# Performance work log

Measured on AMD Instinct MI355X. Metric: run time of the kernel, lower is better.

The kernel has to match this reference:

```python
import jax, jax.numpy as jnp
import numpy as np

N = 131072          # num MCMC chains (num_samples)
N_STEPS = 60        # sample_mcmc default n_steps
EPS_INIT = 10.0     # sample_mcmc default eps_init
H = 128             # hidden width of the energy MLP


def setup_inputs() -> dict:
    key = jax.random.key(0)
    ks = jax.random.split(key, 8)
    d = {}
    # init points uniform in [-1, 1] (mimics the fresh-sample branch / buffer contents)
    d["x0"] = jax.random.uniform(ks[0], (N, 2), jnp.float32, minval=-1.0, maxval=1.0)
    # MLP 2 -> 128 -> 128 -> 128 -> 128 -> 1 (Kaiming-ish scale)
    def init_w(k, shape):
        fan_in = shape[0]
        return jax.random.normal(k, shape, jnp.float32) / jnp.sqrt(jnp.float32(fan_in))
    d["w1"] = init_w(ks[1], (2, H));  d["b1"] = jnp.zeros((H,), jnp.float32)
    d["w2"] = init_w(ks[2], (H, H));  d["b2"] = jnp.zeros((H,), jnp.float32)
    d["w3"] = init_w(ks[3], (H, H));  d["b3"] = jnp.zeros((H,), jnp.float32)
    d["w4"] = init_w(ks[4], (H, H));  d["b4"] = jnp.zeros((H,), jnp.float32)
    d["w5"] = init_w(ks[5], (H, 1));  d["b5"] = jnp.zeros((1,), jnp.float32)
    # pre-drawn Langevin noise for each of the 60 steps (torch.randn_like per step)
    d["noise"] = jax.random.normal(ks[6], (N_STEPS, N, 2), jnp.float32)
    return d


def _energy(x, params):
    # nn.Sequential(Linear, SiLU, Linear, SiLU, Linear, SiLU, Linear, SiLU, Linear)
    w1, b1, w2, b2, w3, b3, w4, b4, w5, b5 = params
    h = jax.nn.silu(x @ w1 + b1)
    h = jax.nn.silu(h @ w2 + b2)
    h = jax.nn.silu(h @ w3 + b3)
    h = jax.nn.silu(h @ w4 + b4)
    return h @ w5 + b5  # [N, 1]


def reference(x0, w1, b1, w2, b2, w3, b3, w4, b4, w5, b5, noise):
    params = (w1, b1, w2, b2, w3, b3, w4, b4, w5, b5)
    # grad of sum of energies wrt x == per-sample dE/dx
    grad_fn = jax.grad(lambda x: _energy(x, params).sum())

    def step(x, inp):
        i, nz = inp
        eps = EPS_INIT * (1.0 - i / N_STEPS)  # eps_init - eps_init*step/n_steps
        # torch.autograd.grad (create_graph=False) -> detached grad
        g = jnp.clip(jax.lax.stop_gradient(grad_fn(x)), -0.03, 0.03)
        x = jnp.clip(x + jnp.sqrt(2.0 * eps) * nz * 0.005 + eps * g, -2.43, 3.05)
        return x, None

    steps = jnp.arange(N_STEPS, dtype=jnp.float32)
    x, _ = jax.lax.scan(step, x0, (steps, noise))
    return x
```

## Files before the change

### kernel.cpp

```cpp
#include <hip/hip_runtime.h>
#include <stdint.h>

#define NTOT    131072
#define NSTEP   60
#define SBLK    32
#define NBLK    (NTOT / SBLK)
#define PLANE_H 16384
#define IMG_H   32768
#define BPLANE_H 4096
#define ACT_H   8192

#define OFF_ACT0 0
#define OFF_ACT1 16384
#define OFF_GP   32768
#define OFF_W1C  33792
#define OFF_B2   35840
#define OFF_B3   36352
#define OFF_B4   36864
#define OFF_W5   37376
#define OFF_XB   37888
#define LDS_TOTAL 38144

typedef float  f32x4  __attribute__((ext_vector_type(4)));
typedef float  f32x16 __attribute__((ext_vector_type(16)));
typedef short  bf16x8 __attribute__((ext_vector_type(8)));
union FragU { bf16x8 v; uint32_t u[4]; uint16_t h[8]; };

static __device__ __forceinline__ uint32_t rne_bits(float f) {
  uint32_t u = __float_as_uint(f);
  return u + 0x7fffu + ((u >> 16) & 1u);
}
static __device__ __forceinline__ float fsigm(float z) {
  return __builtin_amdgcn_rcpf(1.0f + __builtin_amdgcn_exp2f(z * -1.44269504089f));
}
static __device__ __forceinline__ uint32_t cvt_pk_bf16(float a, float b) {
  uint32_t r;
  asm("v_cvt_pk_bf16_f32 %0, %1, %2" : "=v"(r) : "v"(a), "v"(b));
  return r;
}

extern "C" __global__ void ebm_prep_kernel(const float* __restrict__ w2,
                                           const float* __restrict__ w3,
                                           const float* __restrict__ w4,
                                           uint16_t* __restrict__ ws) {
  int img = blockIdx.x;
  bool bwd = img >= 3;
  int li = bwd ? 5 - img : img;
  const float* w = (li == 0) ? w2 : (li == 1) ? w3 : w4;
  uint16_t* hiP = ws + (size_t)img * IMG_H;
  uint16_t* loP = hiP + PLANE_H;
  for (int e = threadIdx.x; e < 16384; e += blockDim.x) {
    int i = e >> 7, o = e & 127;
    int m = bwd ? i : o;
    int k = bwd ? o : i;
    int slot = ((m >> 5) * 8 + (k >> 4)) * 64 + (m & 31) + 32 * ((k >> 3) & 1);
    int off = slot * 8 + (k & 7);
    float v = w[e];
    uint32_t tb = rne_bits(v);
    float lo = v - __uint_as_float(tb & 0xffff0000u);
    hiP[off] = (uint16_t)(tb >> 16);
    loP[off] = (uint16_t)(rne_bits(lo) >> 16);
  }
}

extern "C" __global__ void __launch_bounds__(256, 2)
ebm_mcmc_kernel(const float* __restrict__ x0, const float* __restrict__ w1,
                const float* __restrict__ b1, const float* __restrict__ b2,
                const float* __restrict__ b3, const float* __restrict__ b4,
                const float* __restrict__ w5, const float* __restrict__ noise,
                const uint16_t* __restrict__ wsW, float* __restrict__ out)
{
  extern __shared__ char smem[];
  uint16_t* ACT0  = (uint16_t*)(smem + OFF_ACT0);
  uint16_t* ACT1  = (uint16_t*)(smem + OFF_ACT1);
  float*    GPf   = (float*)(smem + OFF_GP);
  f32x4*    W1C   = (f32x4*)(smem + OFF_W1C);
  float*    B2s   = (float*)(smem + OFF_B2);
  float*    B3s   = (float*)(smem + OFF_B3);
  float*    B4s   = (float*)(smem + OFF_B4);
  float*    W5s   = (float*)(smem + OFF_W5);
  float*    XB    = (float*)(smem + OFF_XB);

  const int t   = threadIdx.x;
  const int blk = blockIdx.x;

  if (t < 128) {
    f32x4 v; v.x = w1[t]; v.y = w1[128 + t]; v.z = b1[t]; v.w = 0.0f;
    W1C[t] = v;
    B2s[t] = b2[t]; B3s[t] = b3[t]; B4s[t] = b4[t]; W5s[t] = w5[t];
  }
  if (t < 64) XB[t] = x0[(size_t)blk * 64 + t];

  const int lane = t & 63;
  const int wave = t >> 6;
  const int c32 = lane & 31;
  const int h   = lane >> 5;
  const int wr  = wave;

  size_t nbase = (size_t)blk * 64 + (t & 63);
  float nz = (t < 64) ? noise[nbase] : 0.0f;

  __syncthreads();

  f32x16 acc;
  float D1[16], D2[16], D3[16];

  auto gemm = [&](int img, const uint16_t* AB) {
    const uint16_t* ab = wsW + (size_t)img * IMG_H + (size_t)(wr * 4096 + lane * 8);
    acc = (f32x16)0.0f;
#pragma unroll
    for (int ks = 0; ks < 8; ++ks) {
      FragU Ah, Al;
      Ah.v = *(const bf16x8*)(ab + ks * 512);
      Al.v = *(const bf16x8*)(ab + ks * 512 + PLANE_H);
      const uint16_t* bp = AB + (ks * 64 + lane) * 8;
      FragU Bh, Bl;
      Bh.v = *(const bf16x8*)bp;
      Bl.v = *(const bf16x8*)(bp + BPLANE_H);
      acc = __builtin_amdgcn_mfma_f32_32x32x16_bf16(Ah.v, Bh.v, acc, 0, 0, 0);
      acc = __builtin_amdgcn_mfma_f32_32x32x16_bf16(Ah.v, Bl.v, acc, 0, 0, 0);
      acc = __builtin_amdgcn_mfma_f32_32x32x16_bf16(Al.v, Bh.v, acc, 0, 0, 0);
    }
  };

  auto storeAct = [&](uint16_t* AB, int tt, f32x4 v) {
    uint32_t h01 = cvt_pk_bf16(v[0], v[1]);
    uint32_t h23 = cvt_pk_bf16(v[2], v[3]);
    float r0 = v[0] - __uint_as_float(h01 << 16);
    float r1 = v[1] - __uint_as_float(h01 & 0xffff0000u);
    float r2 = v[2] - __uint_as_float(h23 << 16);
    float r3 = v[3] - __uint_as_float(h23 & 0xffff0000u);
    int slot = (2 * wr + (tt >> 1)) * 64 + c32 + 32 * (tt & 1);
    uint16_t* p = AB + slot * 8 + 4 * h;
    *(uint2*)p = make_uint2(h01, h23);
    *(uint2*)(p + BPLANE_H) = make_uint2(cvt_pk_bf16(r0, r1), cvt_pk_bf16(r2, r3));
  };

  auto ep_fwd = [&](const float* Bs, float* D, uint16_t* AB) {
#pragma unroll
    for (int tt = 0; tt < 4; ++tt) {
      f32x4 bv = *(const f32x4*)(Bs + 32 * wr + 8 * tt + 4 * h);
      f32x4 hv;
#pragma unroll
      for (int rr = 0; rr < 4; ++rr) {
        float z = acc[4 * tt + rr] + bv[rr];
        float s = fsigm(z);
        float hh = z * s;
        D[4 * tt + rr] = s * (1.0f + z - hh);
        hv[rr] = hh;
      }
      storeAct(AB, tt, hv);
    }
  };

  auto ep_v4 = [&](uint16_t* AB) {
#pragma unroll
    for (int tt = 0; tt < 4; ++tt) {
      f32x4 bv = *(const f32x4*)(B4s + 32 * wr + 8 * tt + 4 * h);
      f32x4 wv = *(const f32x4*)(W5s + 32 * wr + 8 * tt + 4 * h);
      f32x4 vv;
#pragma unroll
      for (int rr = 0; rr < 4; ++rr) {
        float z = acc[4 * tt + rr] + bv[rr];
        float s = fsigm(z);
        vv[rr] = wv[rr] * (s * (1.0f + z - z * s));
      }
      storeAct(AB, tt, vv);
    }
  };

  auto ep_bwd = [&](float* D, uint16_t* AB) {
#pragma unroll
    for (int tt = 0; tt < 4; ++tt) {
      f32x4 vv;
#pragma unroll
      for (int rr = 0; rr < 4; ++rr)
        vv[rr] = acc[4 * tt + rr] * D[4 * tt + rr];
      storeAct(AB, tt, vv);
    }
  };

  auto ep_bwd1 = [&]() {
    float gx = 0.f, gy = 0.f;
#pragma unroll
    for (int tt = 0; tt < 4; ++tt) {
      const f32x4* wp = W1C + 32 * wr + 8 * tt + 4 * h;
#pragma unroll
      for (int rr = 0; rr < 4; ++rr) {
        f32x4 w = wp[rr];
        float v = acc[4 * tt + rr] * D1[4 * tt + rr];
        gx = fmaf(v, w.x, gx);
        gy = fmaf(v, w.y, gy);
      }
    }
    gx += __shfl_xor(gx, 32);
    gy += __shfl_xor(gy, 32);
    if (h == 0) {
      *(float2*)(GPf + (wr * 32 + c32) * 2) = make_float2(gx, gy);
    }
  };

  auto l1_phase = [&](uint16_t* AB) {
    float2 xv = *(const float2*)(XB + 2 * c32);
#pragma unroll
    for (int tt = 0; tt < 4; ++tt) {
      const f32x4* wp = W1C + 32 * wr + 8 * tt + 4 * h;
      f32x4 hv;
#pragma unroll
      for (int rr = 0; rr < 4; ++rr) {
        f32x4 w = wp[rr];
        float z = fmaf(xv.x, w.x, fmaf(xv.y, w.y, w.z));
        float s = fsigm(z);
        float hh = z * s;
        D1[4 * tt + rr] = s * (1.0f + z - hh);
        hv[rr] = hh;
      }
      storeAct(AB, tt, hv);
    }
  };

  auto g_finish = [&](int step) {
    if (t < 64) {
      float g = GPf[t] + GPf[64 + t] + GPf[128 + t] + GPf[192 + t];
      g = fminf(fmaxf(g, -0.03f), 0.03f);
      float epsv = 10.0f * (1.0f - (float)step / 60.0f);
      float xn = XB[t] + sqrtf(2.0f * epsv) * nz * 0.005f + epsv * g;
      xn = fminf(fmaxf(xn, -2.43f), 3.05f);
      XB[t] = xn;
      if (step == NSTEP - 1) {
        out[(size_t)blk * 64 + t] = xn;
      } else {
        nz = noise[(size_t)(step + 1) * NTOT * 2 + nbase];
      }
    }
  };

#pragma unroll 1
  for (int step = 0; step < NSTEP; ++step) {
    l1_phase(ACT0);                 __syncthreads();
    gemm(0, ACT0); ep_fwd(B2s, D2, ACT1); __syncthreads();
    gemm(1, ACT1); ep_fwd(B3s, D3, ACT0); __syncthreads();
    gemm(2, ACT0); ep_v4(ACT1);           __syncthreads();
    gemm(3, ACT1); ep_bwd(D3, ACT0);      __syncthreads();
    gemm(4, ACT0); ep_bwd(D2, ACT1);      __syncthreads();
    gemm(5, ACT1); ep_bwd1();             __syncthreads();
    g_finish(step);                 __syncthreads();
  }
}

extern "C" void kernel_launch(void* const* d_in, const int* in_sizes, int n_in,
                              void* d_out, int out_size, void* d_ws, size_t ws_size,
                              hipStream_t stream) {
  (void)in_sizes; (void)n_in; (void)out_size; (void)ws_size;
  hipFuncSetAttribute((const void*)ebm_mcmc_kernel,
                      hipFuncAttributeMaxDynamicSharedMemorySize, LDS_TOTAL);
  ebm_prep_kernel<<<6, 256, 0, stream>>>(
      (const float*)d_in[3], (const float*)d_in[5], (const float*)d_in[7],
      (uint16_t*)d_ws);
  ebm_mcmc_kernel<<<NBLK, 256, LDS_TOTAL, stream>>>(
      (const float*)d_in[0], (const float*)d_in[1], (const float*)d_in[2],
      (const float*)d_in[4], (const float*)d_in[6], (const float*)d_in[8],
      (const float*)d_in[9], (const float*)d_in[11], (const uint16_t*)d_ws,
      (float*)d_out);
}
```

Before: 5.862 ms.

## Process 64 chains per block so each weight fragment feeds two MFMA tiles

Doubles the samples per block from 32 to 64. Each wave now keeps two accumulator tiles, so every A-fragment (weight) loaded from global memory is reused across two B tiles, which halves weight traffic per sample and the number of blocks. It also recomputes the layer-1 SiLU derivative in the last backward epilogue instead of keeping D1 in registers. In exchange it doubles LDS use and accumulator registers, which may lower occupancy.

Result: slower. 6.268 ms (+6.9%).

```diff
diff --git a/kernel.cpp b/kernel.cpp
--- a/kernel.cpp
+++ b/kernel.cpp
@@ -3,23 +3,22 @@
 
 #define NTOT    131072
 #define NSTEP   60
-#define SBLK    32
+#define SBLK    64
 #define NBLK    (NTOT / SBLK)
 #define PLANE_H 16384
 #define IMG_H   32768
-#define BPLANE_H 4096
-#define ACT_H   8192
+#define BPLANE_H 8192
 
 #define OFF_ACT0 0
-#define OFF_ACT1 16384
-#define OFF_GP   32768
-#define OFF_W1C  33792
-#define OFF_B2   35840
-#define OFF_B3   36352
-#define OFF_B4   36864
-#define OFF_W5   37376
-#define OFF_XB   37888
-#define LDS_TOTAL 38144
+#define OFF_ACT1 32768
+#define OFF_GP   65536
+#define OFF_W1C  67584
+#define OFF_B2   69632
+#define OFF_B3   70144
+#define OFF_B4   70656
+#define OFF_W5   71168
+#define OFF_XB   71680
+#define LDS_TOTAL 72192
 
 typedef float  f32x4  __attribute__((ext_vector_type(4)));
 typedef float  f32x16 __attribute__((ext_vector_type(16)));
@@ -88,8 +87,8 @@
     f32x4 v; v.x = w1[t]; v.y = w1[128 + t]; v.z = b1[t]; v.w = 0.0f;
     W1C[t] = v;
     B2s[t] = b2[t]; B3s[t] = b3[t]; B4s[t] = b4[t]; W5s[t] = w5[t];
+    XB[t] = x0[(size_t)blk * 128 + t];
   }
-  if (t < 64) XB[t] = x0[(size_t)blk * 64 + t];
 
   const int lane = t & 63;
   const int wave = t >> 6;
@@ -97,40 +96,45 @@
   const int h   = lane >> 5;
   const int wr  = wave;
 
-  size_t nbase = (size_t)blk * 64 + (t & 63);
-  float nz = (t < 64) ? noise[nbase] : 0.0f;
+  size_t nbase = (size_t)blk * 128 + (t & 127);
+  float nz = (t < 128) ? noise[nbase] : 0.0f;
 
   __syncthreads();
 
-  f32x16 acc;
-  float D1[16], D2[16], D3[16];
+  f32x16 acc[2];
+  float D2[32], D3[32];
 
   auto gemm = [&](int img, const uint16_t* AB) {
     const uint16_t* ab = wsW + (size_t)img * IMG_H + (size_t)(wr * 4096 + lane * 8);
-    acc = (f32x16)0.0f;
+    acc[0] = (f32x16)0.0f; acc[1] = (f32x16)0.0f;
 #pragma unroll
     for (int ks = 0; ks < 8; ++ks) {
       FragU Ah, Al;
       Ah.v = *(const bf16x8*)(ab + ks * 512);
       Al.v = *(const bf16x8*)(ab + ks * 512 + PLANE_H);
-      const uint16_t* bp = AB + (ks * 64 + lane) * 8;
-      FragU Bh, Bl;
-      Bh.v = *(const bf16x8*)bp;
-      Bl.v = *(const bf16x8*)(bp + BPLANE_H);
-      acc = __builtin_amdgcn_mfma_f32_32x32x16_bf16(Ah.v, Bh.v, acc, 0, 0, 0);
-      acc = __builtin_amdgcn_mfma_f32_32x32x16_bf16(Ah.v, Bl.v, acc, 0, 0, 0);
-      acc = __builtin_amdgcn_mfma_f32_32x32x16_bf16(Al.v, Bh.v, acc, 0, 0, 0);
-    }
-  };
-
-  auto storeAct = [&](uint16_t* AB, int tt, f32x4 v) {
+      const uint16_t* bp0 = AB + ((ks) * 64 + lane) * 8;
+      const uint16_t* bp1 = AB + ((8 * 8 + ks * 64) + lane) * 8;
+      FragU B0h, B0l, B1h, B1l;
+      B0h.v = *(const bf16x8*)bp0;  B0l.v = *(const bf16x8*)(bp0 + BPLANE_H);
+      bp1 = AB + (((8 + ks)) * 64 + lane) * 8;
+      B1h.v = *(const bf16x8*)bp1;  B1l.v = *(const bf16x8*)(bp1 + BPLANE_H);
+      acc[0] = __builtin_amdgcn_mfma_f32_32x32x16_bf16(Ah.v, B0h.v, acc[0], 0, 0, 0);
+      acc[1] = __builtin_amdgcn_mfma_f32_32x32x16_bf16(Ah.v, B1h.v, acc[1], 0, 0, 0);
+      acc[0] = __builtin_amdgcn_mfma_f32_32x32x16_bf16(Ah.v, B0l.v, acc[0], 0, 0, 0);
+      acc[1] = __builtin_amdgcn_mfma_f32_32x32x16_bf16(Ah.v, B1l.v, acc[1], 0, 0, 0);
+      acc[0] = __builtin_amdgcn_mfma_f32_32x32x16_bf16(Al.v, B0h.v, acc[0], 0, 0, 0);
+      acc[1] = __builtin_amdgcn_mfma_f32_32x32x16_bf16(Al.v, B1h.v, acc[1], 0, 0, 0);
+    }
+  };
+
+  auto storeAct = [&](uint16_t* AB, int b, int tt, f32x4 v) {
     uint32_t h01 = cvt_pk_bf16(v[0], v[1]);
     uint32_t h23 = cvt_pk_bf16(v[2], v[3]);
     float r0 = v[0] - __uint_as_float(h01 << 16);
     float r1 = v[1] - __uint_as_float(h01 & 0xffff0000u);
     float r2 = v[2] - __uint_as_float(h23 << 16);
     float r3 = v[3] - __uint_as_float(h23 & 0xffff0000u);
-    int slot = (2 * wr + (tt >> 1)) * 64 + c32 + 32 * (tt & 1);
+    int slot = (b * 8 + 2 * wr + (tt >> 1)) * 64 + c32 + 32 * (tt & 1);
     uint16_t* p = AB + slot * 8 + 4 * h;
     *(uint2*)p = make_uint2(h01, h23);
     *(uint2*)(p + BPLANE_H) = make_uint2(cvt_pk_bf16(r0, r1), cvt_pk_bf16(r2, r3));
@@ -140,16 +144,19 @@
 #pragma unroll
     for (int tt = 0; tt < 4; ++tt) {
       f32x4 bv = *(const f32x4*)(Bs + 32 * wr + 8 * tt + 4 * h);
-      f32x4 hv;
-#pragma unroll
-      for (int rr = 0; rr < 4; ++rr) {
-        float z = acc[4 * tt + rr] + bv[rr];
-        float s = fsigm(z);
-        float hh = z * s;
-        D[4 * tt + rr] = s * (1.0f + z - hh);
-        hv[rr] = hh;
-      }
-      storeAct(AB, tt, hv);
+#pragma unroll
+      for (int b = 0; b < 2; ++b) {
+        f32x4 hv;
+#pragma unroll
+        for (int rr = 0; rr < 4; ++rr) {
+          float z = acc[b][4 * tt + rr] + bv[rr];
+          float s = fsigm(z);
+          float hh = z * s;
+          D[b * 16 + 4 * tt + rr] = s * (1.0f + z - hh);
+          hv[rr] = hh;
+        }
+        storeAct(AB, b, tt, hv);
+      }
     }
   };
 
@@ -158,77 +165,100 @@
     for (int tt = 0; tt < 4; ++tt) {
       f32x4 bv = *(const f32x4*)(B4s + 32 * wr + 8 * tt + 4 * h);
       f32x4 wv = *(const f32x4*)(W5s + 32 * wr + 8 * tt + 4 * h);
-      f32x4 vv;
-#pragma unroll
-      for (int rr = 0; rr < 4; ++rr) {
-        float z = acc[4 * tt + rr] + bv[rr];
-        float s = fsigm(z);
-        vv[rr] = wv[rr] * (s * (1.0f + z - z * s));
-      }
-      storeAct(AB, tt, vv);
+#pragma unroll
+      for (int b = 0; b < 2; ++b) {
+        f32x4 vv;
+#pragma unroll
+        for (int rr = 0; rr < 4; ++rr) {
+          float z = acc[b][4 * tt + rr] + bv[rr];
+          float s = fsigm(z);
+          vv[rr] = wv[rr] * (s * (1.0f + z - z * s));
+        }
+        storeAct(AB, b, tt, vv);
+      }
     }
   };
 
   auto ep_bwd = [&](float* D, uint16_t* AB) {
 #pragma unroll
-    for (int tt = 0; tt < 4; ++tt) {
-      f32x4 vv;
-#pragma unroll
-      for (int rr = 0; rr < 4; ++rr)
-        vv[rr] = acc[4 * tt + rr] * D[4 * tt + rr];
-      storeAct(AB, tt, vv);
-    }
+    for (int tt = 0; tt < 4; ++tt)
+#pragma unroll
+      for (int b = 0; b < 2; ++b) {
+        f32x4 vv;
+#pragma unroll
+        for (int rr = 0; rr < 4; ++rr)
+          vv[rr] = acc[b][4 * tt + rr] * D[b * 16 + 4 * tt + rr];
+        storeAct(AB, b, tt, vv);
+      }
   };
 
   auto ep_bwd1 = [&]() {
-    float gx = 0.f, gy = 0.f;
+    float2 xv0 = *(const float2*)(XB + 2 * c32);
+    float2 xv1 = *(const float2*)(XB + 2 * (32 + c32));
+    float gx[2] = {0.f, 0.f}, gy[2] = {0.f, 0.f};
 #pragma unroll
     for (int tt = 0; tt < 4; ++tt) {
       const f32x4* wp = W1C + 32 * wr + 8 * tt + 4 * h;
 #pragma unroll
       for (int rr = 0; rr < 4; ++rr) {
         f32x4 w = wp[rr];
-        float v = acc[4 * tt + rr] * D1[4 * tt + rr];
-        gx = fmaf(v, w.x, gx);
-        gy = fmaf(v, w.y, gy);
-      }
-    }
-    gx += __shfl_xor(gx, 32);
-    gy += __shfl_xor(gy, 32);
-    if (h == 0) {
-      *(float2*)(GPf + (wr * 32 + c32) * 2) = make_float2(gx, gy);
+#pragma unroll
+        for (int b = 0; b < 2; ++b) {
+          float2 xv = b ? xv1 : xv0;
+          float z = fmaf(xv.x, w.x, fmaf(xv.y, w.y, w.z));
+          float s = fsigm(z);
+          float hh = z * s;
+          float d1 = s * (1.0f + z - hh);
+          float v = acc[b][4 * tt + rr] * d1;
+          gx[b] = fmaf(v, w.x, gx[b]);
+          gy[b] = fmaf(v, w.y, gy[b]);
+        }
+      }
+    }
+#pragma unroll
+    for (int b = 0; b < 2; ++b) {
+      gx[b] += __shfl_xor(gx[b], 32);
+      gy[b] += __shfl_xor(gy[b], 32);
+      if (h == 0) {
+        int s = 32 * b + c32;
+        *(float2*)(GPf + (wr * 64 + s) * 2) = make_float2(gx[b], gy[b]);
+      }
     }
   };
 
   auto l1_phase = [&](uint16_t* AB) {
-    float2 xv = *(const float2*)(XB + 2 * c32);
+    float2 xv0 = *(const float2*)(XB + 2 * c32);
+    float2 xv1 = *(const float2*)(XB + 2 * (32 + c32));
 #pragma unroll
     for (int tt = 0; tt < 4; ++tt) {
       const f32x4* wp = W1C + 32 * wr + 8 * tt + 4 * h;
-      f32x4 hv;
-#pragma unroll
-      for (int rr = 0; rr < 4; ++rr) {
-        f32x4 w = wp[rr];
-        float z = fmaf(xv.x, w.x, fmaf(xv.y, w.y, w.z));
-        float s = fsigm(z);
-        float hh = z * s;
-        D1[4 * tt + rr] = s * (1.0f + z - hh);
-        hv[rr] = hh;
-      }
-      storeAct(AB, tt, hv);
+      f32x4 w0 = wp[0], w1v = wp[1], w2v = wp[2], w3v = wp[3];
+#pragma unroll
+      for (int b = 0; b < 2; ++b) {
+        float2 xv = b ? xv1 : xv0;
+        f32x4 hv;
+        f32x4 wv_[4] = {w0, w1v, w2v, w3v};
+#pragma unroll
+        for (int rr = 0; rr < 4; ++rr) {
+          float z = fmaf(xv.x, wv_[rr].x, fmaf(xv.y, wv_[rr].y, wv_[rr].z));
+          float s = fsigm(z);
+          hv[rr] = z * s;
+        }
+        storeAct(AB, b, tt, hv);
+      }
     }
   };
 
   auto g_finish = [&](int step) {
-    if (t < 64) {
-      float g = GPf[t] + GPf[64 + t] + GPf[128 + t] + GPf[192 + t];
+    if (t < 128) {
+      float g = GPf[t] + GPf[128 + t] + GPf[256 + t] + GPf[384 + t];
       g = fminf(fmaxf(g, -0.03f), 0.03f);
       float epsv = 10.0f * (1.0f - (float)step / 60.0f);
       float xn = XB[t] + sqrtf(2.0f * epsv) * nz * 0.005f + epsv * g;
       xn = fminf(fmaxf(xn, -2.43f), 3.05f);
       XB[t] = xn;
       if (step == NSTEP - 1) {
-        out[(size_t)blk * 64 + t] = xn;
+        out[(size_t)blk * 128 + t] = xn;
       } else {
         nz = noise[(size_t)(step + 1) * NTOT * 2 + nbase];
       }
@@ -237,14 +267,14 @@
 
 #pragma unroll 1
   for (int step = 0; step < NSTEP; ++step) {
-    l1_phase(ACT0);                 __syncthreads();
+    l1_phase(ACT0);                       __syncthreads();
     gemm(0, ACT0); ep_fwd(B2s, D2, ACT1); __syncthreads();
     gemm(1, ACT1); ep_fwd(B3s, D3, ACT0); __syncthreads();
     gemm(2, ACT0); ep_v4(ACT1);           __syncthreads();
     gemm(3, ACT1); ep_bwd(D3, ACT0);      __syncthreads();
     gemm(4, ACT0); ep_bwd(D2, ACT1);      __syncthreads();
     gemm(5, ACT1); ep_bwd1();             __syncthreads();
-    g_finish(step);                 __syncthreads();
+    g_finish(step);                       __syncthreads();
   }
 }
 
```
